# Performance work log

Measured on AMD Instinct MI355X. Metric: run time of the kernel, lower is better.

Reference implementation:

```python
import jax, jax.numpy as jnp
import numpy as np

N_HEAD = 8
D_HEAD = 128   # dim_k = dim_q = dim_v
SEG_LEN = 512
EPS = 1e-6


def setup_inputs() -> dict:
    key = jax.random.key(0)
    ks = jax.random.split(key, 8)
    B, T, D = 2, 4096, 1024
    scale = 0.02
    x = jax.random.normal(ks[0], (B, T, D), dtype=jnp.float32)
    w_q = jax.random.normal(ks[1], (D, N_HEAD * D_HEAD), dtype=jnp.float32) * scale
    w_k = jax.random.normal(ks[2], (D, N_HEAD * D_HEAD), dtype=jnp.float32) * scale
    w_v = jax.random.normal(ks[3], (D, N_HEAD * D_HEAD), dtype=jnp.float32) * scale
    b_q = jnp.zeros((N_HEAD * D_HEAD,), jnp.float32)
    b_k = jnp.zeros((N_HEAD * D_HEAD,), jnp.float32)
    b_v = jnp.zeros((N_HEAD * D_HEAD,), jnp.float32)
    beta = jnp.zeros((N_HEAD,), jnp.float32)
    return {"x": x, "w_q": w_q, "b_q": b_q, "w_k": w_k, "b_k": b_k,
            "w_v": w_v, "b_v": b_v, "beta": beta}


def _heads(y, B, T):
    # [B,T,H*D] -> [B,H,T,D]
    return y.reshape(B, T, N_HEAD, D_HEAD).transpose(0, 2, 1, 3)


def reference(x, w_q, b_q, w_k, b_k, w_v, b_v, beta):
    B, T, _ = x.shape
    S = T // SEG_LEN
    q = _heads(x @ w_q + b_q, B, T)
    k = _heads(x @ w_k + b_k, B, T)
    v = _heads(x @ w_v + b_v, B, T)

    # segment: [B,H,T,D] -> [S,B,H,L,D]
    def seg(y):
        return y.reshape(B, N_HEAD, S, SEG_LEN, D_HEAD).transpose(2, 0, 1, 3, 4)
    qs, ks_, vs = seg(q), seg(k), seg(v)

    causal = jnp.tril(jnp.ones((SEG_LEN, SEG_LEN), bool))
    gate = jax.nn.sigmoid(beta).reshape(1, N_HEAD, 1, 1)
    inv_sqrt_d = 1.0 / jnp.sqrt(jnp.asarray(D_HEAD, x.dtype))

    def step(carry, segdat):
        M, z = carry                      # M: [B,H,Dk,Dv], z: [B,H,Dk]
        qc, kc, vc = segdat               # [B,H,L,D]
        sq = jax.nn.elu(qc) + 1.0
        sk = jax.nn.elu(kc) + 1.0
        # retrieval from memory BEFORE update
        a_mem = jnp.einsum('bhld,bhde->bhle', sq, M) / (
            jnp.einsum('bhld,bhd->bhl', sq, z)[..., None] + EPS)
        # delta-rule memory update
        retr_k = jnp.einsum('bhld,bhde->bhle', sk, M) / (
            jnp.einsum('bhld,bhd->bhl', sk, z)[..., None] + EPS)
        M = M + jnp.einsum('bhld,bhle->bhde', sk, vc - retr_k)
        z = z + sk.sum(axis=2)
        # local causal dot-product attention within the segment
        scores = jnp.einsum('bhld,bhmd->bhlm', qc, kc) * inv_sqrt_d
        scores = jnp.where(causal, scores, jnp.asarray(-1e30, scores.dtype))
        a_dot = jnp.einsum('bhlm,bhmd->bhld', jax.nn.softmax(scores, axis=-1), vc)
        # long-term context injection
        a = gate * a_mem + (1.0 - gate) * a_dot
        return (M, z), a

    M0 = jnp.zeros((B, N_HEAD, D_HEAD, D_HEAD), x.dtype)
    z0 = jnp.zeros((B, N_HEAD, D_HEAD), x.dtype)
    _, out = jax.lax.scan(step, (M0, z0), (qs, ks_, vs))
    # [S,B,H,L,D] -> [B,T,H*D]
    out = out.transpose(1, 3, 0, 2, 4).reshape(B, T, N_HEAD * D_HEAD)
    # wait: axes of out are [S,B,H,L,D]; reorder to [B,S,L,H,D]
    return out


# fix ordering: define reference properly (overrides above draft path)
def reference(x, w_q, b_q, w_k, b_k, w_v, b_v, beta):
    B, T, _ = x.shape
    S = T // SEG_LEN
    q = _heads(x @ w_q + b_q, B, T)
    k = _heads(x @ w_k + b_k, B, T)
    v = _heads(x @ w_v + b_v, B, T)

    def seg(y):
        return y.reshape(B, N_HEAD, S, SEG_LEN, D_HEAD).transpose(2, 0, 1, 3, 4)
    qs, ks_, vs = seg(q), seg(k), seg(v)

    causal = jnp.tril(jnp.ones((SEG_LEN, SEG_LEN), bool))
    gate = jax.nn.sigmoid(beta).reshape(1, N_HEAD, 1, 1)
    inv_sqrt_d = 1.0 / jnp.sqrt(jnp.asarray(D_HEAD, x.dtype))

    def step(carry, segdat):
        M, z = carry
        qc, kc, vc = segdat
        sq = jax.nn.elu(qc) + 1.0
        sk = jax.nn.elu(kc) + 1.0
        a_mem = jnp.einsum('bhld,bhde->bhle', sq, M) / (
            jnp.einsum('bhld,bhd->bhl', sq, z)[..., None] + EPS)
        retr_k = jnp.einsum('bhld,bhde->bhle', sk, M) / (
            jnp.einsum('bhld,bhd->bhl', sk, z)[..., None] + EPS)
        M = M + jnp.einsum('bhld,bhle->bhde', sk, vc - retr_k)
        z = z + sk.sum(axis=2)
        scores = jnp.einsum('bhld,bhmd->bhlm', qc, kc) * inv_sqrt_d
        scores = jnp.where(causal, scores, jnp.asarray(-1e30, scores.dtype))
        a_dot = jnp.einsum('bhlm,bhmd->bhld', jax.nn.softmax(scores, axis=-1), vc)
        a = gate * a_mem + (1.0 - gate) * a_dot
        return (M, z), a

    M0 = jnp.zeros((B, N_HEAD, D_HEAD, D_HEAD), x.dtype)
    z0 = jnp.zeros((B, N_HEAD, D_HEAD), x.dtype)
    _, out = jax.lax.scan(step, (M0, z0), (qs, ks_, vs))  # [S,B,H,L,D]
    out = out.transpose(1, 0, 3, 2, 4).reshape(B, T, N_HEAD * D_HEAD)
    return out
```

## Files before the change

kernel.cpp:

```cpp
#include <hip/hip_runtime.h>
#include <hip/hip_bf16.h>

typedef __attribute__((ext_vector_type(8))) short bf16x8;
typedef __attribute__((ext_vector_type(4))) float f32x4;
typedef unsigned short u16;
typedef unsigned int u32;

#define DEV static __device__ __forceinline__

DEV float bf2f(u16 u){ u32 x = ((u32)u)<<16; float f; __builtin_memcpy(&f,&x,4); return f; }
DEV u16 f2bf(float f){ u32 x; __builtin_memcpy(&x,&f,4); return (u16)((x + 0x7fffu + ((x>>16)&1u))>>16); }
DEV float elu1(float x){ return x > 0.f ? x + 1.f : __expf(x); }

DEV void gload16(const u16* g, u16* l){
  __builtin_amdgcn_global_load_lds(
      (const __attribute__((address_space(1))) unsigned int*)(g),
      (__attribute__((address_space(3))) unsigned int*)(l), 16, 0, 0);
}

#define MFMA(a,b,c) __builtin_amdgcn_mfma_f32_16x16x32_bf16((a),(b),(c),0,0,0)

#define NB 2
#define NT 4096
#define NH 8
#define DH 128
#define NS 8
#define SL 512
#define ND 1024
#define N3 3072
#define EPS 1e-6f

__global__ __launch_bounds__(256) void k_xc(const float* __restrict__ x, u16* __restrict__ xb){
  int i = blockIdx.x*256 + threadIdx.x;
  const float4 v0 = *(const float4*)(x + (size_t)i*8);
  const float4 v1 = *(const float4*)(x + (size_t)i*8 + 4);
  bf16x8 o;
  o[0]=(short)f2bf(v0.x); o[1]=(short)f2bf(v0.y); o[2]=(short)f2bf(v0.z); o[3]=(short)f2bf(v0.w);
  o[4]=(short)f2bf(v1.x); o[5]=(short)f2bf(v1.y); o[6]=(short)f2bf(v1.z); o[7]=(short)f2bf(v1.w);
  *(bf16x8*)(xb + (size_t)i*8) = o;
}

__global__ __launch_bounds__(256) void k_wt(const float* __restrict__ wq,
                                            const float* __restrict__ wk,
                                            const float* __restrict__ wv,
                                            u16* __restrict__ wt,
                                            float* __restrict__ cs){
  __shared__ float t[32][33];
  const int z = blockIdx.z;
  const float* w = (z==0) ? wq : (z==1 ? wk : wv);
  const int k0 = blockIdx.x*32, n0 = blockIdx.y*32;
  const int tx = threadIdx.x, ty = threadIdx.y;
  if (z==0 && blockIdx.x==0 && blockIdx.y==0){
    const int tid = ty*32 + tx;
#pragma unroll
    for (int i=0;i<64;i++) cs[tid + i*256] = 0.f;
  }
#pragma unroll
  for (int i=0;i<4;i++) t[ty+i*8][tx] = w[(size_t)(k0+ty+i*8)*ND + n0+tx];
  __syncthreads();
#pragma unroll
  for (int i=0;i<4;i++)
    wt[(size_t)(z*ND + n0+ty+i*8)*ND + k0+tx] = f2bf(t[tx][ty+i*8]);
}

__global__ __launch_bounds__(256) void k_gemm(const u16* __restrict__ xb,
                                              const u16* __restrict__ wt,
                                              const float* __restrict__ bq,
                                              const float* __restrict__ bk,
                                              const float* __restrict__ bv,
                                              u16* __restrict__ qkv,
                                              u16* __restrict__ pkTo,
                                              u16* __restrict__ vto,
                                              float* __restrict__ cs){
  __shared__ __align__(16) u16 As[128*64];
  __shared__ __align__(16) u16 Bs[128*64];
  const int m0 = blockIdx.x*128, n0 = blockIdx.y*128;
  const int tid = threadIdx.x;
  const int w = tid>>6, lane = tid&63, g = lane>>4, li = lane&15;
  const int wr = w>>1, wc = w&1;
  const int srow = lane>>3;
  const int ssl  = (lane&7) ^ srow;
  f32x4 z4 = {0.f,0.f,0.f,0.f};
  f32x4 acc[4][4];
#pragma unroll
  for (int mi=0;mi<4;mi++)
#pragma unroll
    for (int ni=0;ni<4;ni++) acc[mi][ni] = z4;

  for (int kt=0; kt<16; ++kt){
    const int k0 = kt*64;
#pragma unroll
    for (int i=0;i<4;i++){
      const int c = i*4 + w;
      const int row = c*8 + srow;
      gload16(xb + (size_t)(m0+row)*ND + k0 + ssl*8, As + c*512);
      gload16(wt + (size_t)(n0+row)*ND + k0 + ssl*8, Bs + c*512);
    }
    __syncthreads();
#pragma unroll
    for (int kk=0;kk<2;kk++){
      bf16x8 a[4], bb[4];
#pragma unroll
      for (int mi=0;mi<4;mi++){
        int row = wr*64 + mi*16 + li;
        int slot = kk*4 + g;
        a[mi] = *(const bf16x8*)(As + row*64 + ((slot^(row&7))<<3));
      }
#pragma unroll
      for (int ni=0;ni<4;ni++){
        int row = wc*64 + ni*16 + li;
        int slot = kk*4 + g;
        bb[ni] = *(const bf16x8*)(Bs + row*64 + ((slot^(row&7))<<3));
      }
#pragma unroll
      for (int mi=0;mi<4;mi++)
#pragma unroll
        for (int ni=0;ni<4;ni++)
          acc[mi][ni] = MFMA(a[mi], bb[ni], acc[mi][ni]);
    }
    __syncthreads();
  }

  const int part = n0 >> 10;
  const int hh = (n0 >> 7) & 7;
  const int bb2 = m0 >> 12;
  const int tloc = m0 & (NT-1);
  const int rb = lane>>3, cb = lane&7;
  u16* SCw = (w < 2 ? As : Bs) + (w&1)*4096;

  if (part < 2){
#pragma unroll
    for (int ni=0;ni<4;ni++){
      const int n = n0 + wc*64 + ni*16 + li;
      const float bias = (part==0) ? bq[n] : bk[n-ND];
#pragma unroll
      for (int mi=0;mi<4;mi++)
#pragma unroll
        for (int rr=0;rr<4;rr++){
          const int ml = mi*16 + 4*g + rr;
          const int nl = ni*16 + li;
          SCw[ml*64 + (((nl>>3)^(ml&7))<<3) + (nl&7)] = f2bf(acc[mi][ni][rr] + bias);
        }
    }
    __syncthreads();
#pragma unroll
    for (int j=0;j<8;j++){
      const int r = j*8 + rb;
      bf16x8 v = *(const bf16x8*)(SCw + r*64 + ((cb^(r&7))<<3));
      *(bf16x8*)(qkv + (size_t)(m0 + wr*64 + r)*N3 + n0 + wc*64 + cb*8) = v;
    }
  }
  if (part >= 1){
    __syncthreads();
    float csum[4] = {0.f,0.f,0.f,0.f};
#pragma unroll
    for (int ni=0;ni<4;ni++){
      const int n = n0 + wc*64 + ni*16 + li;
      const float bias = (part==1) ? bk[n-ND] : bv[n-2*ND];
      const int nl = ni*16 + li;
#pragma unroll
      for (int mi=0;mi<4;mi++){
        float v0 = acc[mi][ni][0] + bias;
        float v1 = acc[mi][ni][1] + bias;
        float v2 = acc[mi][ni][2] + bias;
        float v3 = acc[mi][ni][3] + bias;
        if (part==1){
          v0 = elu1(v0); v1 = elu1(v1); v2 = elu1(v2); v3 = elu1(v3);
          csum[ni] += v0+v1+v2+v3;
        }
        short4 pk;
        pk.x = (short)f2bf(v0); pk.y = (short)f2bf(v1);
        pk.z = (short)f2bf(v2); pk.w = (short)f2bf(v3);
        const int gran = (2*mi + (g>>1)) ^ (nl&7) ^ (((li>>3)&1)<<2);
        *(short4*)(SCw + nl*64 + (gran<<3) + 4*(g&1)) = pk;
      }
    }
    __syncthreads();
    u16* dstT = (part==1) ? pkTo : vto;
    const int bh = bb2*8 + hh;
#pragma unroll
    for (int j=0;j<8;j++){
      const int r = j*8 + rb;
      bf16x8 v = *(const bf16x8*)(SCw + r*64 + ((cb ^ (r&7) ^ ((j&1)<<2))<<3));
      *(bf16x8*)(dstT + (size_t)(bh*DH + wc*64 + r)*NT + tloc + wr*64 + cb*8) = v;
    }
    if (part==1){
      const int s = tloc >> 9;
      const int bhs = bb2*64 + hh*8 + s;
#pragma unroll
      for (int ni=0;ni<4;ni++){
        float c = csum[ni];
        c += __shfl_xor(c,16); c += __shfl_xor(c,32);
        if (g==0)
          atomicAdd(&cs[(size_t)bhs*DH + wc*64 + ni*16 + li], c);
      }
    }
  }
}

__global__ __launch_bounds__(512) void k_dinv(const u16* __restrict__ qkv,
                                              const float* __restrict__ cs,
                                              float* __restrict__ dinvK){
  const int bhs = blockIdx.x, half = blockIdx.y;
  const int b = bhs>>6, h = (bhs>>3)&7, s = bhs&7;
  const int tid = threadIdx.x, w = tid>>6, lane = tid&63, grp = lane>>4, li = lane&15;
  __shared__ float zl[128];
  if (tid < 128){
    float a = 0.f;
    for (int sp=0; sp<s; ++sp) a += cs[(size_t)(bhs - s + sp)*DH + tid];
    zl[tid] = a;
  }
  __syncthreads();
#pragma unroll
  for (int it=0; it<8; ++it){
    const int r = half*256 + w*32 + it*4 + grp;
    bf16x8 v = *(const bf16x8*)(qkv + (size_t)(b*NT + s*SL + r)*N3 + ND + h*DH + li*8);
    float p = 0.f;
#pragma unroll
    for (int j=0;j<8;j++) p += elu1(bf2f((u16)v[j])) * zl[li*8+j];
    p += __shfl_xor(p,1); p += __shfl_xor(p,2);
    p += __shfl_xor(p,4); p += __shfl_xor(p,8);
    if (li == 0) dinvK[(size_t)bhs*SL + r] = 1.f/(p + EPS);
  }
}

__global__ __launch_bounds__(512) void k_gram(const u16* __restrict__ pkT,
                                              const u16* __restrict__ vtb,
                                              const float* __restrict__ dinvK,
                                              u16* __restrict__ G, float* __restrict__ Bm){
  const int bhs = blockIdx.x, ec = blockIdx.y;
  const int bh = bhs>>3, s = bhs&7, tb = s*SL;
  const int tid = threadIdx.x, w = tid>>6, lane = tid&63, g = lane>>4, li = lane&15;
  __shared__ __align__(16) u16 Bk[32*512];
  __shared__ __align__(16) u16 Bv[32*512];
  __shared__ float dv[512];
  dv[tid] = dinvK[(size_t)bhs*SL + tid];
#pragma unroll
  for (int i=0;i<4;i++){
    const int ee = i*8 + w;
    const size_t rowo = ((size_t)bh*DH + ec*32 + ee)*NT + tb + ((lane^w)<<3);
    gload16(pkT + rowo, Bk + ee*512);
    gload16(vtb + rowo, Bv + ee*512);
  }
  __syncthreads();
  f32x4 z4 = {0.f,0.f,0.f,0.f};
  f32x4 Ga[2] = {z4,z4}, Ba[2] = {z4,z4};
  const u16* arow = pkT + ((size_t)bh*DH + 16*w + li)*NT + tb;
  for (int ks=0; ks<16; ++ks){
    const int r0 = ks*32 + g*8;
    bf16x8 araw = *(const bf16x8*)(arow + r0);
    float4 d0 = *(const float4*)(dv + r0);
    float4 d1 = *(const float4*)(dv + r0 + 4);
    bf16x8 ascl;
    ascl[0] = (short)f2bf(bf2f((u16)araw[0]) * d0.x);
    ascl[1] = (short)f2bf(bf2f((u16)araw[1]) * d0.y);
    ascl[2] = (short)f2bf(bf2f((u16)araw[2]) * d0.z);
    ascl[3] = (short)f2bf(bf2f((u16)araw[3]) * d0.w);
    ascl[4] = (short)f2bf(bf2f((u16)araw[4]) * d1.x);
    ascl[5] = (short)f2bf(bf2f((u16)araw[5]) * d1.y);
    ascl[6] = (short)f2bf(bf2f((u16)araw[6]) * d1.z);
    ascl[7] = (short)f2bf(bf2f((u16)araw[7]) * d1.w);
    const int slot = ks*4 + g;
#pragma unroll
    for (int ni=0;ni<2;ni++){
      const int ee = ni*16 + li;
      bf16x8 bk8 = *(const bf16x8*)(Bk + ee*512 + ((slot^(li&7))<<3));
      bf16x8 bv8 = *(const bf16x8*)(Bv + ee*512 + ((slot^(li&7))<<3));
      Ga[ni] = MFMA(ascl, bk8, Ga[ni]);
      Ba[ni] = MFMA(araw, bv8, Ba[ni]);
    }
  }
#pragma unroll
  for (int ni=0;ni<2;ni++)
#pragma unroll
    for (int rr=0;rr<4;rr++){
      const int dd = 16*w + 4*g + rr;
      const int ee = ec*32 + ni*16 + li;
      G[((size_t)bhs*DH + dd)*DH + ee] = f2bf(Ga[ni][rr]);
      Bm[((size_t)bhs*DH + dd)*DH + ee] = Ba[ni][rr];
    }
}

__global__ __launch_bounds__(512) void k_scan(const u16* __restrict__ G,
                                              const float* __restrict__ Bm,
                                              u16* __restrict__ MTs){
  const int bh = blockIdx.x, ec = blockIdx.y;
  const int tid = threadIdx.x, w = tid>>6, lane = tid&63, g = lane>>4, li = lane&15;
  __shared__ float MF[16*132];
  __shared__ __align__(16) u16 MB[16*128];
  for (int i = tid; i < 16*132; i += 512) MF[i] = 0.f;
  __syncthreads();
  const int dr = w*16 + li;
  for (int s=0;s<NS;s++){
    const size_t bhs = (size_t)bh*NS + s;
    if (tid < 256){
      const int e = tid>>4, dg = tid&15;
      const float* src = MF + e*132 + dg*8;
      bf16x8 v;
#pragma unroll
      for (int j=0;j<8;j++) v[j] = (short)f2bf(src[j]);
      *(bf16x8*)(MTs + bhs*16384 + (size_t)(ec*16+e)*128 + dg*8) = v;
      *(bf16x8*)(MB + e*128 + ((dg^(e&7))<<3)) = v;
    }
    __syncthreads();
    f32x4 acc = {0.f,0.f,0.f,0.f};
#pragma unroll
    for (int ks=0;ks<4;ks++){
      bf16x8 a = *(const bf16x8*)(G + ((size_t)bhs*DH + dr)*DH + ks*32 + g*8);
      const int sl = ks*4 + g;
      bf16x8 bfr = *(const bf16x8*)(MB + li*128 + ((sl^(li&7))<<3));
      acc = MFMA(a, bfr, acc);
    }
#pragma unroll
    for (int rr=0;rr<4;rr++){
      const int d = w*16 + 4*g + rr;
      const float delta = Bm[((size_t)bhs*DH + d)*DH + ec*16 + li] - acc[rr];
      MF[li*132 + d] += delta;
    }
    __syncthreads();
  }
}

__global__ __launch_bounds__(512) void k_attn(const u16* __restrict__ qkv,
                                              const u16* __restrict__ vtb,
                                              const u16* __restrict__ MTs,
                                              const float* __restrict__ cs,
                                              const float* __restrict__ beta,
                                              float* __restrict__ out){
  const int bhs = blockIdx.x, half = blockIdx.y;
  const int b = bhs>>6, h = (bhs>>3)&7, s = bhs&7, bh = bhs>>3;
  const int tid = threadIdx.x, w = tid>>6, lane = tid&63, g = lane>>4, li = lane&15;
  const int jq = (w < 4) ? (half + 2*w) : (15 - half - 2*(w-4));
  const int qb = jq*32;
  const float gate = 1.f/(1.f + __expf(-beta[h]));
  const float SCL = 0.08838834764831845f * 1.4426950408889634f;
  __shared__ __align__(16) u16 P[8*1024];
  __shared__ float zl[128];
  __shared__ float dinvW[8][32];
  u16* Pw = P + w*1024;

  if (tid < 128){
    float a = 0.f;
    for (int sp=0; sp<s; ++sp) a += cs[(size_t)(bhs - s + sp)*DH + tid];
    zl[tid] = a;
  }
  __syncthreads();

  {
    const int r = qb + (lane&31);
    const int dh = (lane>>5)*64;
    const u16* qrow = qkv + (size_t)(b*NT + s*SL + r)*N3 + h*DH + dh;
    float p = 0.f;
#pragma unroll
    for (int j=0;j<64;j+=8){
      bf16x8 v = *(const bf16x8*)(qrow + j);
#pragma unroll
      for (int t=0;t<8;t++) p += elu1(bf2f((u16)v[t])) * zl[dh + j + t];
    }
    p += __shfl_xor(p, 32);
    if (lane < 32) dinvW[w][lane] = 1.f/(p + EPS);
  }

  bf16x8 qf[2][4];
#pragma unroll
  for (int mf=0; mf<2; ++mf)
#pragma unroll
    for (int kf=0; kf<4; ++kf)
      qf[mf][kf] = *(const bf16x8*)(qkv + (size_t)(b*NT + s*SL + qb + mf*16 + li)*N3 + h*DH + kf*32 + g*8);

  bf16x8 one8;
#pragma unroll
  for (int j=0;j<8;j++) one8[j] = (short)0x3F80;

  f32x4 z4 = {0.f,0.f,0.f,0.f};
  f32x4 O[2][8];
  f32x4 lsum[2] = {z4, z4};
#pragma unroll
  for (int mf=0;mf<2;++mf)
#pragma unroll
    for (int nf=0;nf<8;++nf) O[mf][nf] = z4;

  const int nch = jq + 1;
  for (int c=0; c<nch; ++c){
    const int kb = c*32;
    f32x4 sa[2][2];
#pragma unroll
    for (int mf=0;mf<2;++mf)
#pragma unroll
      for (int nf=0;nf<2;++nf) sa[mf][nf] = z4;
#pragma unroll
    for (int kf=0; kf<4; ++kf)
#pragma unroll
      for (int nf=0; nf<2; ++nf){
        bf16x8 bk8 = *(const bf16x8*)(qkv + (size_t)(b*NT + s*SL + kb + nf*16 + li)*N3 + ND + h*DH + kf*32 + g*8);
        sa[0][nf] = MFMA(qf[0][kf], bk8, sa[0][nf]);
        sa[1][nf] = MFMA(qf[1][kf], bk8, sa[1][nf]);
      }
#pragma unroll
    for (int mf=0;mf<2;++mf)
#pragma unroll
      for (int nf=0;nf<2;++nf)
#pragma unroll
        for (int rr=0;rr<4;++rr){
          const int row = qb + mf*16 + 4*g + rr, col = kb + nf*16 + li;
          const float p = (col > row) ? 0.f : exp2f(sa[mf][nf][rr]*SCL);
          const int rl = mf*16 + 4*g + rr, cl = nf*16 + li;
          Pw[rl*32 + (((cl>>3)^(rl&3))<<3) + (cl&7)] = f2bf(p);
        }
    bf16x8 pa[2];
#pragma unroll
    for (int mf=0;mf<2;++mf){
      const int row = mf*16 + li;
      pa[mf] = *(const bf16x8*)(Pw + row*32 + ((g^(row&3))<<3));
    }
#pragma unroll
    for (int nf=0;nf<8;++nf){
      bf16x8 bv8 = *(const bf16x8*)(vtb + ((size_t)bh*DH + nf*16 + li)*NT + s*SL + kb + g*8);
      O[0][nf] = MFMA(pa[0], bv8, O[0][nf]);
      O[1][nf] = MFMA(pa[1], bv8, O[1][nf]);
    }
    lsum[0] = MFMA(pa[0], one8, lsum[0]);
    lsum[1] = MFMA(pa[1], one8, lsum[1]);
  }

  f32x4 Am[2][8];
#pragma unroll
  for (int mf=0;mf<2;++mf)
#pragma unroll
    for (int nf=0;nf<8;++nf) Am[mf][nf] = z4;
#pragma unroll
  for (int ks=0;ks<4;++ks){
    bf16x8 pq[2];
#pragma unroll
    for (int mf=0;mf<2;++mf){
      bf16x8 raw = qf[mf][ks];
#pragma unroll
      for (int j=0;j<8;j++) raw[j] = (short)f2bf(elu1(bf2f((u16)raw[j])));
      pq[mf] = raw;
    }
#pragma unroll
    for (int nf=0;nf<8;++nf){
      bf16x8 bfr = *(const bf16x8*)(MTs + ((size_t)bhs*DH + nf*16 + li)*DH + ks*32 + g*8);
      Am[0][nf] = MFMA(pq[0], bfr, Am[0][nf]);
      Am[1][nf] = MFMA(pq[1], bfr, Am[1][nf]);
    }
  }

  const float og = 1.f - gate;
#pragma unroll
  for (int mf=0;mf<2;++mf)
#pragma unroll
    for (int rr=0;rr<4;++rr){
      const int row = qb + mf*16 + 4*g + rr;
      const float invd = og / lsum[mf][rr];
      const float dv = gate * dinvW[w][row - qb];
#pragma unroll
      for (int nf=0;nf<8;++nf)
        out[(size_t)(b*NT + s*SL + row)*ND + h*DH + nf*16 + li] =
            O[mf][nf][rr]*invd + Am[mf][nf][rr]*dv;
    }
}

extern "C" void kernel_launch(void* const* d_in, const int* in_sizes, int n_in,
                              void* d_out, int out_size, void* d_ws, size_t ws_size,
                              hipStream_t stream) {
  (void)in_sizes; (void)n_in; (void)out_size; (void)ws_size;
  const float* x    = (const float*)d_in[0];
  const float* wq   = (const float*)d_in[1];
  const float* bq   = (const float*)d_in[2];
  const float* wk   = (const float*)d_in[3];
  const float* bk   = (const float*)d_in[4];
  const float* wv   = (const float*)d_in[5];
  const float* bv   = (const float*)d_in[6];
  const float* beta = (const float*)d_in[7];
  float* out = (float*)d_out;
  char* ws = (char*)d_ws;

  u16*   wt  = (u16*)  (ws + 0);
  u16*   qkv = (u16*)  (ws + 6291456);
  u16*   vt  = (u16*)  (ws + 56623104);
  u16*   pkT = (u16*)  (ws + 73400320);
  u16*   G   = (u16*)  (ws + 90177536);
  float* Bm  = (float*)(ws + 94371840);
  u16*   MTs = (u16*)  (ws + 102760448);
  float* cs  = (float*)(ws + 106954752);
  float* dinvK = (float*)(ws + 107020288);
  u16*   xb  = (u16*)  (ws + 90177536);

  hipLaunchKernelGGL(k_xc,    dim3(4096),    dim3(256),  0, stream, x, xb);
  hipLaunchKernelGGL(k_wt,    dim3(32,32,3), dim3(32,8), 0, stream, wq, wk, wv, wt, cs);
  hipLaunchKernelGGL(k_gemm,  dim3(64,24),   dim3(256),  0, stream, xb, wt, bq, bk, bv, qkv, pkT, vt, cs);
  hipLaunchKernelGGL(k_dinv,  dim3(128,2),   dim3(512),  0, stream, qkv, cs, dinvK);
  hipLaunchKernelGGL(k_gram,  dim3(128,4),   dim3(512),  0, stream, pkT, vt, dinvK, G, Bm);
  hipLaunchKernelGGL(k_scan,  dim3(16,8),    dim3(512),  0, stream, G, Bm, MTs);
  hipLaunchKernelGGL(k_attn,  dim3(128,2),   dim3(512),  0, stream, qkv, vt, MTs, cs, beta, out);
}
```

Before: 176.4 us.

## Double-buffer LDS tiles in QKV GEMM to overlap global loads with MFMA

The projection GEMM now uses two LDS buffers per operand and prefetches the next k-tile via global_load_lds before computing the current one. It waits with a partial vmcnt and raw s_barrier instead of __syncthreads, so load latency can overlap with MFMA work. This doubles the LDS footprint to 64KB per block, which may reduce occupancy. The transpose-store swizzle in the epilogue is also simplified by dropping an extra XOR term, which changes the LDS bank-conflict pattern.

```diff
diff --git a/kernel.cpp b/kernel.cpp
--- a/kernel.cpp
+++ b/kernel.cpp
@@ -72,8 +72,8 @@
                                               u16* __restrict__ pkTo,
                                               u16* __restrict__ vto,
                                               float* __restrict__ cs){
-  __shared__ __align__(16) u16 As[128*64];
-  __shared__ __align__(16) u16 Bs[128*64];
+  __shared__ __align__(16) u16 As[2][128*64];
+  __shared__ __align__(16) u16 Bs[2][128*64];
   const int m0 = blockIdx.x*128, n0 = blockIdx.y*128;
   const int tid = threadIdx.x;
   const int w = tid>>6, lane = tid&63, g = lane>>4, li = lane&15;
@@ -87,16 +87,27 @@
 #pragma unroll
     for (int ni=0;ni<4;ni++) acc[mi][ni] = z4;
 
+#define STAGE(kt_) do{                                                          \
+    const int k0_ = (kt_)*64;                                                   \
+    u16* A_ = (u16*)As[(kt_)&1];                                                \
+    u16* B_ = (u16*)Bs[(kt_)&1];                                                \
+    _Pragma("unroll")                                                           \
+    for (int i_=0;i_<4;i_++){                                                   \
+      const int c_ = i_*4 + w;                                                  \
+      const int row_ = c_*8 + srow;                                             \
+      gload16(xb + (size_t)(m0+row_)*ND + k0_ + ssl*8, A_ + c_*512);            \
+      gload16(wt + (size_t)(n0+row_)*ND + k0_ + ssl*8, B_ + c_*512);            \
+    }                                                                           \
+  }while(0)
+
+  STAGE(0);
   for (int kt=0; kt<16; ++kt){
-    const int k0 = kt*64;
-#pragma unroll
-    for (int i=0;i<4;i++){
-      const int c = i*4 + w;
-      const int row = c*8 + srow;
-      gload16(xb + (size_t)(m0+row)*ND + k0 + ssl*8, As + c*512);
-      gload16(wt + (size_t)(n0+row)*ND + k0 + ssl*8, Bs + c*512);
-    }
-    __syncthreads();
+    if (kt < 15){ STAGE(kt+1); asm volatile("s_waitcnt vmcnt(8)" ::: "memory"); }
+    else        {              asm volatile("s_waitcnt vmcnt(0)" ::: "memory"); }
+    __builtin_amdgcn_s_barrier();
+    __builtin_amdgcn_sched_barrier(0);
+    const u16* Ab = (const u16*)As[kt&1];
+    const u16* Bb = (const u16*)Bs[kt&1];
 #pragma unroll
     for (int kk=0;kk<2;kk++){
       bf16x8 a[4], bb[4];
@@ -104,13 +115,13 @@
       for (int mi=0;mi<4;mi++){
         int row = wr*64 + mi*16 + li;
         int slot = kk*4 + g;
-        a[mi] = *(const bf16x8*)(As + row*64 + ((slot^(row&7))<<3));
+        a[mi] = *(const bf16x8*)(Ab + row*64 + ((slot^(row&7))<<3));
       }
 #pragma unroll
       for (int ni=0;ni<4;ni++){
         int row = wc*64 + ni*16 + li;
         int slot = kk*4 + g;
-        bb[ni] = *(const bf16x8*)(Bs + row*64 + ((slot^(row&7))<<3));
+        bb[ni] = *(const bf16x8*)(Bb + row*64 + ((slot^(row&7))<<3));
       }
 #pragma unroll
       for (int mi=0;mi<4;mi++)
@@ -118,15 +129,18 @@
         for (int ni=0;ni<4;ni++)
           acc[mi][ni] = MFMA(a[mi], bb[ni], acc[mi][ni]);
     }
-    __syncthreads();
-  }
+    __builtin_amdgcn_sched_barrier(0);
+    __builtin_amdgcn_s_barrier();
+    __builtin_amdgcn_sched_barrier(0);
+  }
+#undef STAGE
 
   const int part = n0 >> 10;
   const int hh = (n0 >> 7) & 7;
   const int bb2 = m0 >> 12;
   const int tloc = m0 & (NT-1);
   const int rb = lane>>3, cb = lane&7;
-  u16* SCw = (w < 2 ? As : Bs) + (w&1)*4096;
+  u16* SCw = (w < 2 ? (u16*)As[0] : (u16*)Bs[0]) + (w&1)*4096;
 
   if (part < 2){
 #pragma unroll
@@ -171,7 +185,7 @@
         short4 pk;
         pk.x = (short)f2bf(v0); pk.y = (short)f2bf(v1);
         pk.z = (short)f2bf(v2); pk.w = (short)f2bf(v3);
-        const int gran = (2*mi + (g>>1)) ^ (nl&7) ^ (((li>>3)&1)<<2);
+        const int gran = (2*mi + (g>>1)) ^ (nl&7);
         *(short4*)(SCw + nl*64 + (gran<<3) + 4*(g&1)) = pk;
       }
     }
@@ -181,7 +195,7 @@
 #pragma unroll
     for (int j=0;j<8;j++){
       const int r = j*8 + rb;
-      bf16x8 v = *(const bf16x8*)(SCw + r*64 + ((cb ^ (r&7) ^ ((j&1)<<2))<<3));
+      bf16x8 v = *(const bf16x8*)(SCw + r*64 + ((cb^(r&7))<<3));
       *(bf16x8*)(dstT + (size_t)(bh*DH + wc*64 + r)*NT + tloc + wr*64 + cb*8) = v;
     }
     if (part==1){
```

Result: faster. 171.7 us (-2.7%).
